# Kernel tuning notes

Measured on AMD Instinct MI355X. Metric: run time of the kernel, lower is better.

## Reference

```python
import jax, jax.numpy as jnp
import numpy as np

MAX_DISP = 4  # init kwarg


def setup_inputs() -> dict:
    key = jax.random.key(0)
    k1, k2 = jax.random.split(key)
    x_1 = jax.random.normal(k1, (8, 128, 128, 128), dtype=jnp.float32)
    x_2 = jax.random.normal(k2, (8, 128, 128, 128), dtype=jnp.float32)
    return {"x_1": x_1, "x_2": x_2}


def reference(x_1, x_2):
    d = MAX_DISP
    H, W = x_1.shape[2], x_1.shape[3]
    # zero-pad x_2 by max_disp on both spatial dims (ConstantPad2d)
    x2p = jnp.pad(x_2, ((0, 0), (0, 0), (d, d), (d, d)))
    # loop over the fixed (2d+1)^2 = 81 displacement offsets (structural, not data dim)
    outs = [
        jnp.mean(x_1 * x2p[:, :, dx:dx + H, dy:dy + W], axis=1)  # [B,H,W]
        for dx in range(2 * d + 1)
        for dy in range(2 * d + 1)
    ]
    return jnp.stack(outs, axis=1)  # [B, 81, H, W]
```

## Files before the change

kernel.cpp:

```cpp
#include <hip/hip_runtime.h>


constexpr int Bn = 8, Cn = 128, Hn = 128, Wn = 128;
constexpr int HWn = Hn * Wn;
constexpr int TH = 4;
constexpr int NDH = 3;
constexpr int NR = TH + NDH - 1;
constexpr int WP = 144;
constexpr int NF4 = (NR * 140) / 4;

__global__ __launch_bounds__(256, 3)
void corr_kernel(const float* __restrict__ x1, const float* __restrict__ x2,
                 float* __restrict__ out) {
  __shared__ float s2[2][NR][WP];
  __shared__ float sred[128][36];

  const int t    = threadIdx.x;
  const int half = t >> 7;
  const int q    = t & 127;
  const int row  = q >> 5;
  const int w0   = (q & 31) << 2;

  const int bx   = blockIdx.x;
  const int g    = bx % 3;
  const int tile = bx / 3;
  const int b    = tile >> 5;
  const int h0   = (tile & 31) * TH;
  const int dhm  = g * NDH - 4;

  const int i0 = q, i1 = q + 128;
  const int sr0 = i0 / 35, fc0 = i0 % 35;
  int sr1 = i1 / 35; const int fc1 = i1 % 35;
  const bool act1 = (i1 < NF4);
  if (sr1 > NR - 1) sr1 = NR - 1;
  const int gr0 = h0 + dhm + sr0;
  const int gr1 = h0 + dhm + sr1;
  const bool ok0 = ((unsigned)gr0 < (unsigned)Hn) && (fc0 >= 1) && (fc0 <= 32);
  const bool ok1 = act1 && ((unsigned)gr1 < (unsigned)Hn) && (fc1 >= 1) && (fc1 <= 32);
  const int off0 = gr0 * Wn + fc0 * 4 - 4;
  const int off1 = gr1 * Wn + fc1 * 4 - 4;
  float* lp0 = &s2[half][sr0][fc0 * 4];
  float* lp1 = &s2[half][sr1][fc1 * 4];

  const float* x1c = x1 + (size_t)b * Cn * HWn + (size_t)(half * 64) * HWn
                        + (h0 + row) * Wn + w0;
  const float* x2c = x2 + (size_t)b * Cn * HWn + (size_t)(half * 64) * HWn;

  float4 acc[NDH][9];
#pragma unroll
  for (int r = 0; r < NDH; ++r)
#pragma unroll
    for (int dw = 0; dw < 9; ++dw) acc[r][dw] = make_float4(0.f, 0.f, 0.f, 0.f);

#pragma unroll 1
  for (int cc = 0; cc < 64; ++cc) {
    const float4 a = *(const float4*)x1c;
    float4 v0 = make_float4(0.f, 0.f, 0.f, 0.f);
    float4 v1 = make_float4(0.f, 0.f, 0.f, 0.f);
    if (ok0) v0 = *(const float4*)(x2c + off0);
    if (ok1) v1 = *(const float4*)(x2c + off1);
    *(float4*)lp0 = v0;
    if (act1) *(float4*)lp1 = v1;
    __syncthreads();

#pragma unroll
    for (int r = 0; r < NDH; ++r) {
      const float* srow = &s2[half][row + r][w0];
      const float4 wa = *(const float4*)(srow);
      const float4 wb = *(const float4*)(srow + 4);
      const float4 wc = *(const float4*)(srow + 8);
      const float win[12] = {wa.x, wa.y, wa.z, wa.w, wb.x, wb.y, wb.z, wb.w,
                             wc.x, wc.y, wc.z, wc.w};
#pragma unroll
      for (int dw = 0; dw < 9; ++dw) {
        acc[r][dw].x += a.x * win[dw + 0];
        acc[r][dw].y += a.y * win[dw + 1];
        acc[r][dw].z += a.z * win[dw + 2];
        acc[r][dw].w += a.w * win[dw + 3];
      }
    }
    x1c += HWn;
    x2c += HWn;
    __syncthreads();
  }

  const float scale = 1.0f / 128.0f;
  float* ob = out + (size_t)b * 81 * HWn + (size_t)(h0 + row) * Wn + w0;
#pragma unroll
  for (int r = 0; r < NDH; ++r) {
    if (half) {
#pragma unroll
      for (int dw = 0; dw < 9; ++dw) *(float4*)&sred[q][dw * 4] = acc[r][dw];
    }
    __syncthreads();
    if (!half) {
      const int obase = (g * 3 + r) * 9;
#pragma unroll
      for (int dw = 0; dw < 9; ++dw) {
        const float4 s = *(const float4*)&sred[q][dw * 4];
        const float4 m = acc[r][dw];
        float4 rz;
        rz.x = (m.x + s.x) * scale;
        rz.y = (m.y + s.y) * scale;
        rz.z = (m.z + s.z) * scale;
        rz.w = (m.w + s.w) * scale;
        *(float4*)(ob + (size_t)(obase + dw) * HWn) = rz;
      }
    }
    __syncthreads();
  }
}

extern "C" void kernel_launch(void* const* d_in, const int* in_sizes, int n_in,
                              void* d_out, int out_size, void* d_ws, size_t ws_size,
                              hipStream_t stream) {
  const float* x1 = (const float*)d_in[0];
  const float* x2 = (const float*)d_in[1];
  float* out = (float*)d_out;
  const int n_wgs = Bn * (Hn / TH) * 3;
  corr_kernel<<<dim3(n_wgs), dim3(256), 0, stream>>>(x1, x2, out);
}
```

Measured before the change: 205.1 us.

## Double-buffer shared tiles with register prefetch and remap blocks per XCD

Each channel's x1 and x2 values are now prefetched into registers one iteration ahead, and x2 tiles alternate between two shared-memory buffers. This removes one barrier per channel step and lets global loads overlap compute. Blocks are also remapped so the three displacement groups of a tile, and neighbouring tiles, land on the same XCD, which should improve L2 reuse of x1 and x2 rows. The cost is twice the shared memory for s2 and extra live registers, which could lower occupancy.

```diff
diff --git a/kernel.cpp b/kernel.cpp
--- a/kernel.cpp
+++ b/kernel.cpp
@@ -12,7 +12,7 @@
 __global__ __launch_bounds__(256, 3)
 void corr_kernel(const float* __restrict__ x1, const float* __restrict__ x2,
                  float* __restrict__ out) {
-  __shared__ float s2[2][NR][WP];
+  __shared__ float s2[2][2][NR][WP];
   __shared__ float sred[128][36];
 
   const int t    = threadIdx.x;
@@ -21,9 +21,12 @@
   const int row  = q >> 5;
   const int w0   = (q & 31) << 2;
 
-  const int bx   = blockIdx.x;
-  const int g    = bx % 3;
-  const int tile = bx / 3;
+  const int phys = blockIdx.x;
+  const int xcd  = phys & 7;
+  const int slot = phys >> 3;
+  const int tl   = slot / 3;
+  const int g    = slot % 3;
+  const int tile = xcd * 32 + tl;
   const int b    = tile >> 5;
   const int h0   = (tile & 31) * TH;
   const int dhm  = g * NDH - 4;
@@ -39,8 +42,6 @@
   const bool ok1 = act1 && ((unsigned)gr1 < (unsigned)Hn) && (fc1 >= 1) && (fc1 <= 32);
   const int off0 = gr0 * Wn + fc0 * 4 - 4;
   const int off1 = gr1 * Wn + fc1 * 4 - 4;
-  float* lp0 = &s2[half][sr0][fc0 * 4];
-  float* lp1 = &s2[half][sr1][fc1 * 4];
 
   const float* x1c = x1 + (size_t)b * Cn * HWn + (size_t)(half * 64) * HWn
                         + (h0 + row) * Wn + w0;
@@ -52,20 +53,29 @@
 #pragma unroll
     for (int dw = 0; dw < 9; ++dw) acc[r][dw] = make_float4(0.f, 0.f, 0.f, 0.f);
 
+  float4 pv0 = make_float4(0.f, 0.f, 0.f, 0.f);
+  float4 pv1 = make_float4(0.f, 0.f, 0.f, 0.f);
+  if (ok0) pv0 = *(const float4*)(x2c + off0);
+  if (ok1) pv1 = *(const float4*)(x2c + off1);
+  float4 pa = *(const float4*)x1c;
+
 #pragma unroll 1
   for (int cc = 0; cc < 64; ++cc) {
-    const float4 a = *(const float4*)x1c;
-    float4 v0 = make_float4(0.f, 0.f, 0.f, 0.f);
-    float4 v1 = make_float4(0.f, 0.f, 0.f, 0.f);
-    if (ok0) v0 = *(const float4*)(x2c + off0);
-    if (ok1) v1 = *(const float4*)(x2c + off1);
-    *(float4*)lp0 = v0;
-    if (act1) *(float4*)lp1 = v1;
+    const int buf = cc & 1;
+    *(float4*)&s2[buf][half][sr0][fc0 * 4] = pv0;
+    if (act1) *(float4*)&s2[buf][half][sr1][fc1 * 4] = pv1;
+    const float4 a = pa;
+    if (cc < 63) {
+      const float* nx2 = x2c + (size_t)(cc + 1) * HWn;
+      if (ok0) pv0 = *(const float4*)(nx2 + off0);
+      if (ok1) pv1 = *(const float4*)(nx2 + off1);
+      pa = *(const float4*)(x1c + (size_t)(cc + 1) * HWn);
+    }
     __syncthreads();
 
 #pragma unroll
     for (int r = 0; r < NDH; ++r) {
-      const float* srow = &s2[half][row + r][w0];
+      const float* srow = &s2[buf][half][row + r][w0];
       const float4 wa = *(const float4*)(srow);
       const float4 wb = *(const float4*)(srow + 4);
       const float4 wc = *(const float4*)(srow + 8);
@@ -79,9 +89,6 @@
         acc[r][dw].w += a.w * win[dw + 3];
       }
     }
-    x1c += HWn;
-    x2c += HWn;
-    __syncthreads();
   }
 
   const float scale = 1.0f / 128.0f;
```

New measurement: 189.1 us. 1.08x faster.
